# Kernel tuning notes

Measured on AMD Instinct MI355X. Metric: run time of the kernel, lower is better.

Reference implementation:

```python
import jax, jax.numpy as jnp
import numpy as np

C = 256
E = C // 2  # embed_dim = in_channels / 2


def setup_inputs() -> dict:
    key = jax.random.key(0)
    ks = jax.random.split(key, 9)
    B, H, W = 8, 64, 64
    x = jax.random.normal(ks[0], (B, C, H, W), dtype=jnp.float32)
    s_in = 1.0 / np.sqrt(C)
    s_e = 1.0 / np.sqrt(E)
    wq = jax.random.uniform(ks[1], (E, C), jnp.float32, -s_in, s_in)
    bq = jax.random.uniform(ks[2], (E,), jnp.float32, -s_in, s_in)
    wk = jax.random.uniform(ks[3], (E, C), jnp.float32, -s_in, s_in)
    bk = jax.random.uniform(ks[4], (E,), jnp.float32, -s_in, s_in)
    wv = jax.random.uniform(ks[5], (E, C), jnp.float32, -s_in, s_in)
    bv = jax.random.uniform(ks[6], (E,), jnp.float32, -s_in, s_in)
    wo = jax.random.uniform(ks[7], (C, E), jnp.float32, -s_e, s_e)
    bo = jax.random.uniform(ks[8], (C,), jnp.float32, -s_e, s_e)
    return {"x": x, "wq": wq, "bq": bq, "wk": wk, "bk": bk,
            "wv": wv, "bv": bv, "wo": wo, "bo": bo}


def reference(x, wq, bq, wk, bk, wv, bv, wo, bo):
    B, Cc, H, W = x.shape
    N = H * W
    # flatten spatial: [B, N, C]; 1x1 conv == per-pixel linear over channels
    xf = x.reshape(B, Cc, N).transpose(0, 2, 1)
    q = jnp.einsum('bnc,ec->bne', xf, wq) + bq   # [B, N, E]
    k = jnp.einsum('bnc,ec->bne', xf, wk) + bk   # [B, N, E]
    v = jnp.einsum('bnc,ec->bne', xf, wv) + bv   # [B, N, E]
    attn_score = jnp.einsum('bne,bme->bnm', q, k)  # [B, N, N]
    attn_prob = jax.nn.softmax(attn_score, axis=-1)
    feat = jnp.einsum('bnm,bme->bne', attn_prob, v)  # [B, N, E]
    out = jnp.einsum('bne,ce->bnc', feat, wo) + bo   # expansion 1x1 conv
    out = out.transpose(0, 2, 1).reshape(B, Cc, H, W)
    return out + x
```

## Files before the change

kernel.cpp:

```cpp
#include <hip/hip_runtime.h>
#include <hip/hip_bf16.h>


typedef __attribute__((ext_vector_type(8))) short s16x8;
typedef __attribute__((ext_vector_type(4))) short s16x4;
typedef __attribute__((ext_vector_type(4))) float f32x4;

#define B_ 8
#define C_ 256
#define E_ 128
#define N_ 4096
#define SLICES 4
#define SLICE_KV (N_ / SLICES)
#define NTILES (SLICE_KV / 64)
#define PST 76
#define LOG2E 1.44269504f
#define SHIFT2 21.6404256f

#define GLDS16(g, l) __builtin_amdgcn_global_load_lds( \
    (const __attribute__((address_space(1))) void*)(g), \
    (__attribute__((address_space(3))) void*)(l), 16, 0, 0)

static __device__ __forceinline__ unsigned short f2bf(float f) {
    union { float f; unsigned int u; } v; v.f = f;
    return (unsigned short)((v.u + 0x7FFFu + ((v.u >> 16) & 1u)) >> 16);
}
static __device__ __forceinline__ float bf2f(unsigned short h) {
    union { unsigned int u; float f; } v; v.u = ((unsigned int)h) << 16;
    return v.f;
}

__global__ __launch_bounds__(256) void convert_w(
    const float* __restrict__ wq, const float* __restrict__ wk,
    const float* __restrict__ wv, const float* __restrict__ wo,
    unsigned short* __restrict__ wqb, unsigned short* __restrict__ wkb,
    unsigned short* __restrict__ wvb, unsigned short* __restrict__ wob)
{
    const int i = blockIdx.x * 256 + threadIdx.x;
    wqb[i] = f2bf(wq[i]);
    wkb[i] = f2bf(wk[i]);
    wvb[i] = f2bf(wv[i]);
    wob[i] = f2bf(wo[i]);
}

__global__ __launch_bounds__(256, 2) void qkv_kernel(
    const float* __restrict__ x,
    const unsigned short* __restrict__ wqb, const float* __restrict__ bq,
    const unsigned short* __restrict__ wkb, const float* __restrict__ bk,
    const unsigned short* __restrict__ wvb, const float* __restrict__ bv,
    unsigned short* __restrict__ Q, unsigned short* __restrict__ K,
    unsigned short* __restrict__ Vt)
{
    __shared__ unsigned short xs[64 * 264];

    const int tid = threadIdx.x;
    const int b  = blockIdx.x >> 6;
    const int n0 = (blockIdx.x & 63) << 6;

    {
        const int n  = tid & 63;
        const int c0 = tid >> 6;
        const float* xp = x + ((size_t)(b * C_) << 12) + n0 + n;
        for (int it = 0; it < 64; ++it) {
            const int c = it * 4 + c0;
            xs[n * 264 + c] = f2bf(xp[(size_t)c << 12]);
        }
    }
    __syncthreads();

    const int w = tid >> 6, l = tid & 63, hi = l >> 4, lx = l & 15;

    for (int idx = w; idx < 24; idx += 4) {
        const int out = idx >> 3;
        const int et  = idx & 7;
        const int e0  = et << 4;
        const unsigned short* W = (out == 0) ? wqb : (out == 1) ? wkb : wvb;
        const float* bias = (out == 0) ? bq : (out == 1) ? bk : bv;
        const float scale = (out == 0) ? LOG2E : 1.0f;

        s16x8 af[8];
        const unsigned short* wp = W + (e0 + lx) * C_ + hi * 8;
#pragma unroll
        for (int ks = 0; ks < 8; ++ks) af[ks] = *(const s16x8*)(wp + ks * 32);

        float bi[4];
#pragma unroll
        for (int r = 0; r < 4; ++r) bi[r] = bias[e0 + hi * 4 + r];

#pragma unroll
        for (int nt = 0; nt < 4; ++nt) {
            f32x4 acc = {0.f, 0.f, 0.f, 0.f};
#pragma unroll
            for (int ks = 0; ks < 8; ++ks) {
                s16x8 xb = *(const s16x8*)&xs[(nt * 16 + lx) * 264 + ks * 32 + hi * 8];
                acc = __builtin_amdgcn_mfma_f32_16x16x32_bf16(af[ks], xb, acc, 0, 0, 0);
            }
            const int n = n0 + nt * 16 + lx;
            if (out < 2) {
                unsigned short* dst =
                    ((out == 0) ? Q : K) + ((size_t)(b * N_ + n) << 7) + e0 + hi * 4;
                s16x4 pk;
#pragma unroll
                for (int r = 0; r < 4; ++r) pk[r] = (short)f2bf((acc[r] + bi[r]) * scale);
                *(s16x4*)dst = pk;
            } else {
#pragma unroll
                for (int r = 0; r < 4; ++r)
                    Vt[((size_t)(b * E_ + e0 + hi * 4 + r) << 12) + n] =
                        f2bf(acc[r] + bi[r]);
            }
        }
    }
}

__global__ __launch_bounds__(256, 2) void attn_partial(
    const unsigned short* __restrict__ Q, const unsigned short* __restrict__ K,
    const unsigned short* __restrict__ Vt,
    unsigned short* __restrict__ featP, float* __restrict__ denomP)
{
    __shared__ unsigned short Kx[64 * 128];
    __shared__ unsigned short Vs[128 * 64];
    __shared__ unsigned short Ps[4][32 * PST];

    const int tid = threadIdx.x;
    const int b   = blockIdx.x & 7;
    const int idx = blockIdx.x >> 3;
    const int sl  = idx >> 5;
    const int qt  = idx & 31;
    const int w = tid >> 6, l = tid & 63, hi = l >> 4, lx = l & 15;
    const int q0 = qt * 128 + w * 32;

    s16x8 qA[2][4];
#pragma unroll
    for (int qf = 0; qf < 2; ++qf) {
        const unsigned short* qp =
            Q + ((size_t)(b * N_ + q0 + qf * 16 + lx) << 7) + hi * 8;
#pragma unroll
        for (int ks = 0; ks < 4; ++ks) qA[qf][ks] = *(const s16x8*)(qp + ks * 32);
    }

    f32x4 feat[2][8];
#pragma unroll
    for (int qf = 0; qf < 2; ++qf)
#pragma unroll
        for (int ef = 0; ef < 8; ++ef) feat[qf][ef] = (f32x4){0.f, 0.f, 0.f, 0.f};
    float dAcc[8];
#pragma unroll
    for (int i = 0; i < 8; ++i) dAcc[i] = 0.f;

    const unsigned short* Kg = K + ((size_t)(b * N_) << 7);
    const unsigned short* Vg = Vt + ((size_t)(b * E_) << 12);
    unsigned short* pw = &Ps[w][0];


    for (int it = 0; it < NTILES; ++it) {
        const int kv0 = sl * SLICE_KV + it * 64;
        __syncthreads();
#pragma unroll
        for (int i = 0; i < 4; ++i) {
            const int flat = tid + i * 256;
            const int row = flat >> 4, c16 = flat & 15;
            GLDS16(Kg + (size_t)(kv0 + row) * 128 + ((c16 ^ (row & 7)) << 3),
                   &Kx[(i * 256 + w * 64) << 3]);
        }
#pragma unroll
        for (int i = 0; i < 4; ++i) {
            const int flat = tid + i * 256;
            const int e = flat >> 3, c8 = flat & 7;
            GLDS16(Vg + (((size_t)e << 12) + kv0) + ((c8 ^ (e & 7)) << 3),
                   &Vs[(i * 256 + w * 64) << 3]);
        }
        __syncthreads();

#pragma unroll
        for (int kvf = 0; kvf < 4; ++kvf) {
            f32x4 s0 = {0.f, 0.f, 0.f, 0.f}, s1 = {0.f, 0.f, 0.f, 0.f};
#pragma unroll
            for (int ks = 0; ks < 4; ++ks) {
                s16x8 kb = *(const s16x8*)&Kx[((kvf * 16 + lx) << 7) +
                                              (((ks * 4 + hi) ^ (lx & 7)) << 3)];
                s0 = __builtin_amdgcn_mfma_f32_16x16x32_bf16(qA[0][ks], kb, s0, 0, 0, 0);
                s1 = __builtin_amdgcn_mfma_f32_16x16x32_bf16(qA[1][ks], kb, s1, 0, 0, 0);
            }
#pragma unroll
            for (int r = 0; r < 4; ++r) {
                float p0 = __builtin_exp2f(s0[r] - SHIFT2);
                float p1 = __builtin_exp2f(s1[r] - SHIFT2);
                dAcc[r]     += p0;
                dAcc[4 + r] += p1;
                pw[(hi * 4 + r) * PST      + kvf * 16 + lx] = f2bf(p0);
                pw[(16 + hi * 4 + r) * PST + kvf * 16 + lx] = f2bf(p1);
            }
        }
#pragma unroll
        for (int ks = 0; ks < 2; ++ks) {
            s16x8 pa0 = *(const s16x8*)&pw[(lx)      * PST + ks * 32 + hi * 8];
            s16x8 pa1 = *(const s16x8*)&pw[(16 + lx) * PST + ks * 32 + hi * 8];
#pragma unroll
            for (int ef = 0; ef < 8; ++ef) {
                s16x8 vb = *(const s16x8*)&Vs[((ef * 16 + lx) << 6) +
                                              (((ks * 4 + hi) ^ (lx & 7)) << 3)];
                feat[0][ef] = __builtin_amdgcn_mfma_f32_16x16x32_bf16(pa0, vb, feat[0][ef], 0, 0, 0);
                feat[1][ef] = __builtin_amdgcn_mfma_f32_16x16x32_bf16(pa1, vb, feat[1][ef], 0, 0, 0);
            }
        }
    }

#pragma unroll
    for (int i = 0; i < 8; ++i) {
        float v = dAcc[i];
        v += __shfl_xor(v, 1); v += __shfl_xor(v, 2);
        v += __shfl_xor(v, 4); v += __shfl_xor(v, 8);
        dAcc[i] = v;
    }
    const size_t qg = (size_t)((sl * 8 + b) * N_ + q0);
    if (lx == 0) {
        float* dP = denomP + qg;
#pragma unroll
        for (int qf = 0; qf < 2; ++qf)
#pragma unroll
            for (int r = 0; r < 4; ++r)
                dP[qf * 16 + hi * 4 + r] = dAcc[qf * 4 + r];
    }
    unsigned short* fP = featP + (qg << 7);
#pragma unroll
    for (int qf = 0; qf < 2; ++qf)
#pragma unroll
        for (int ef = 0; ef < 8; ++ef)
#pragma unroll
            for (int r = 0; r < 4; ++r)
                fP[(qf * 16 + hi * 4 + r) * 128 + ef * 16 + lx] =
                    f2bf(feat[qf][ef][r]);
}

__global__ __launch_bounds__(256, 2) void combine_kernel(
    const unsigned short* __restrict__ featP, const float* __restrict__ denomP,
    const unsigned short* __restrict__ wob, const float* __restrict__ bo,
    const float* __restrict__ x, float* __restrict__ out)
{
    __shared__ unsigned short fs[64 * 136];

    const int tid = threadIdx.x;
    const int b  = blockIdx.x & 7;
    const int nt = blockIdx.x >> 3;

    {
        const int q = tid >> 2, eb = (tid & 3) * 32;
        const int n = nt * 64 + q;
        float den = 0.f;
#pragma unroll
        for (int s = 0; s < SLICES; ++s)
            den += denomP[(size_t)((s * 8 + b) * N_) + n];
        const float inv = 1.f / den;
#pragma unroll
        for (int e8 = 0; e8 < 4; ++e8) {
            float acc[8];
#pragma unroll
            for (int j = 0; j < 8; ++j) acc[j] = 0.f;
#pragma unroll
            for (int s = 0; s < SLICES; ++s) {
                s16x8 v = *(const s16x8*)(featP +
                    (((size_t)((s * 8 + b) * N_) + n) << 7) + eb + e8 * 8);
#pragma unroll
                for (int j = 0; j < 8; ++j) acc[j] += bf2f((unsigned short)v[j]);
            }
            s16x8 o;
#pragma unroll
            for (int j = 0; j < 8; ++j) o[j] = (short)f2bf(acc[j] * inv);
            *(s16x8*)&fs[q * 136 + eb + e8 * 8] = o;
        }
    }
    __syncthreads();

    const int w = tid >> 6, l = tid & 63, hi = l >> 4, lx = l & 15;

    s16x8 fa[4];
#pragma unroll
    for (int ks = 0; ks < 4; ++ks)
        fa[ks] = *(const s16x8*)&fs[(w * 16 + lx) * 136 + ks * 32 + hi * 8];

    const int n = nt * 64 + w * 16 + lx;
    const float* xb = x + ((size_t)(b * C_) << 12);
    float* ob = out + ((size_t)(b * C_) << 12);
#pragma unroll 1
    for (int ct = 0; ct < 16; ++ct) {
        const unsigned short* wp = wob + (ct * 16 + lx) * 128 + hi * 8;
        f32x4 acc = {0.f, 0.f, 0.f, 0.f};
#pragma unroll
        for (int ks = 0; ks < 4; ++ks) {
            s16x8 wb = *(const s16x8*)(wp + ks * 32);
            acc = __builtin_amdgcn_mfma_f32_16x16x32_bf16(wb, fa[ks], acc, 0, 0, 0);
        }
#pragma unroll
        for (int r = 0; r < 4; ++r) {
            const int c = ct * 16 + hi * 4 + r;
            const size_t off = ((size_t)c << 12) + n;
            ob[off] = acc[r] + bo[c] + xb[off];
        }
    }
}

extern "C" void kernel_launch(void* const* d_in, const int* in_sizes, int n_in,
                              void* d_out, int out_size, void* d_ws, size_t ws_size,
                              hipStream_t stream) {
    (void)in_sizes; (void)n_in; (void)out_size; (void)ws_size;
    const float* x  = (const float*)d_in[0];
    const float* wq = (const float*)d_in[1];
    const float* bq = (const float*)d_in[2];
    const float* wk = (const float*)d_in[3];
    const float* bk = (const float*)d_in[4];
    const float* wv = (const float*)d_in[5];
    const float* bv = (const float*)d_in[6];
    const float* wo = (const float*)d_in[7];
    const float* bo = (const float*)d_in[8];

    unsigned short* Q  = (unsigned short*)d_ws;
    unsigned short* K  = Q + (size_t)B_ * N_ * E_;
    unsigned short* Vt = K + (size_t)B_ * N_ * E_;
    unsigned short* featP = Vt + (size_t)B_ * N_ * E_;
    float* denomP = (float*)(featP + (size_t)SLICES * B_ * N_ * E_);
    unsigned short* wqb = (unsigned short*)(denomP + (size_t)SLICES * B_ * N_);
    unsigned short* wkb = wqb + E_ * C_;
    unsigned short* wvb = wkb + E_ * C_;
    unsigned short* wob = wvb + E_ * C_;

    convert_w<<<dim3(128), dim3(256), 0, stream>>>(
        wq, wk, wv, wo, wqb, wkb, wvb, wob);
    qkv_kernel<<<dim3(B_ * (N_ / 64)), dim3(256), 0, stream>>>(
        x, wqb, bq, wkb, bk, wvb, bv, Q, K, Vt);
    attn_partial<<<dim3(B_ * 32 * SLICES), dim3(256), 0, stream>>>(
        Q, K, Vt, featP, denomP);
    combine_kernel<<<dim3(B_ * 64), dim3(256), 0, stream>>>(
        featP, denomP, wob, bo, x, (float*)d_out);
}
```

Baseline: 175.8 us.

## Double-buffer K/V tiles via register prefetch and swizzle P scratch layout

Replaces the direct global-to-LDS loads, which sat behind two barriers per tile, with register prefetch of the next K/V tile into a second LDS buffer. The goal is to overlap global memory latency with the QK and PV MFMA work, leaving one barrier per iteration. The padded P scratch (stride 76) is also replaced by a dense stride-64 layout with an XOR swizzle to avoid bank conflicts. The cost is double the K/V LDS footprint and extra vector registers for the prefetch, which may hurt occupancy at two blocks per CU.

```diff
diff --git a/kernel.cpp b/kernel.cpp
--- a/kernel.cpp
+++ b/kernel.cpp
@@ -13,13 +13,8 @@
 #define SLICES 4
 #define SLICE_KV (N_ / SLICES)
 #define NTILES (SLICE_KV / 64)
-#define PST 76
 #define LOG2E 1.44269504f
 #define SHIFT2 21.6404256f
-
-#define GLDS16(g, l) __builtin_amdgcn_global_load_lds( \
-    (const __attribute__((address_space(1))) void*)(g), \
-    (__attribute__((address_space(3))) void*)(l), 16, 0, 0)
 
 static __device__ __forceinline__ unsigned short f2bf(float f) {
     union { float f; unsigned int u; } v; v.f = f;
@@ -118,9 +113,9 @@
     const unsigned short* __restrict__ Vt,
     unsigned short* __restrict__ featP, float* __restrict__ denomP)
 {
-    __shared__ unsigned short Kx[64 * 128];
-    __shared__ unsigned short Vs[128 * 64];
-    __shared__ unsigned short Ps[4][32 * PST];
+    __shared__ unsigned short Ks[2][64 * 128];
+    __shared__ unsigned short Vs[2][128 * 64];
+    __shared__ unsigned short Ps[4][32 * 64];
 
     const int tid = threadIdx.x;
     const int b   = blockIdx.x & 7;
@@ -152,57 +147,91 @@
     const unsigned short* Vg = Vt + ((size_t)(b * E_) << 12);
     unsigned short* pw = &Ps[w][0];
 
+    const int kRow[4] = { tid >> 4, (tid + 256) >> 4, (tid + 512) >> 4, (tid + 768) >> 4 };
+    const int kC16 = tid & 15;
+    const int vE[4]  = { tid >> 3, (tid + 256) >> 3, (tid + 512) >> 3, (tid + 768) >> 3 };
+    const int vC8 = tid & 7;
+
+    s16x8 nk[4], nv[4];
+    {
+        const int kv0 = sl * SLICE_KV;
+#pragma unroll
+        for (int i = 0; i < 4; ++i)
+            nk[i] = *(const s16x8*)(Kg + (size_t)(kv0 + kRow[i]) * 128 + kC16 * 8);
+#pragma unroll
+        for (int i = 0; i < 4; ++i)
+            nv[i] = *(const s16x8*)(Vg + ((size_t)vE[i] << 12) + kv0 + vC8 * 8);
+#pragma unroll
+        for (int i = 0; i < 4; ++i)
+            *(s16x8*)&Ks[0][kRow[i] * 128 + ((kC16 ^ (kRow[i] & 7)) << 3)] = nk[i];
+#pragma unroll
+        for (int i = 0; i < 4; ++i)
+            *(s16x8*)&Vs[0][vE[i] * 64 + ((vC8 ^ (vE[i] & 7)) << 3)] = nv[i];
+    }
+    __syncthreads();
 
     for (int it = 0; it < NTILES; ++it) {
-        const int kv0 = sl * SLICE_KV + it * 64;
-        __syncthreads();
-#pragma unroll
-        for (int i = 0; i < 4; ++i) {
-            const int flat = tid + i * 256;
-            const int row = flat >> 4, c16 = flat & 15;
-            GLDS16(Kg + (size_t)(kv0 + row) * 128 + ((c16 ^ (row & 7)) << 3),
-                   &Kx[(i * 256 + w * 64) << 3]);
-        }
-#pragma unroll
-        for (int i = 0; i < 4; ++i) {
-            const int flat = tid + i * 256;
-            const int e = flat >> 3, c8 = flat & 7;
-            GLDS16(Vg + (((size_t)e << 12) + kv0) + ((c8 ^ (e & 7)) << 3),
-                   &Vs[(i * 256 + w * 64) << 3]);
-        }
-        __syncthreads();
-
+        const int cur = it & 1;
+        const bool pf = (it + 1 < NTILES);
+        if (pf) {
+            const int kvn = sl * SLICE_KV + (it + 1) * 64;
+#pragma unroll
+            for (int i = 0; i < 4; ++i)
+                nk[i] = *(const s16x8*)(Kg + (size_t)(kvn + kRow[i]) * 128 + kC16 * 8);
+#pragma unroll
+            for (int i = 0; i < 4; ++i)
+                nv[i] = *(const s16x8*)(Vg + ((size_t)vE[i] << 12) + kvn + vC8 * 8);
+        }
+
+        const unsigned short* kxb = &Ks[cur][0];
 #pragma unroll
         for (int kvf = 0; kvf < 4; ++kvf) {
+            s16x8 kb[4];
+#pragma unroll
+            for (int ks = 0; ks < 4; ++ks)
+                kb[ks] = *(const s16x8*)&kxb[(kvf * 16 + lx) * 128 +
+                                             (((ks * 4 + hi) ^ (lx & 7)) << 3)];
             f32x4 s0 = {0.f, 0.f, 0.f, 0.f}, s1 = {0.f, 0.f, 0.f, 0.f};
 #pragma unroll
             for (int ks = 0; ks < 4; ++ks) {
-                s16x8 kb = *(const s16x8*)&Kx[((kvf * 16 + lx) << 7) +
-                                              (((ks * 4 + hi) ^ (lx & 7)) << 3)];
-                s0 = __builtin_amdgcn_mfma_f32_16x16x32_bf16(qA[0][ks], kb, s0, 0, 0, 0);
-                s1 = __builtin_amdgcn_mfma_f32_16x16x32_bf16(qA[1][ks], kb, s1, 0, 0, 0);
+                s0 = __builtin_amdgcn_mfma_f32_16x16x32_bf16(qA[0][ks], kb[ks], s0, 0, 0, 0);
+                s1 = __builtin_amdgcn_mfma_f32_16x16x32_bf16(qA[1][ks], kb[ks], s1, 0, 0, 0);
             }
 #pragma unroll
             for (int r = 0; r < 4; ++r) {
+                const int key = ((hi * 4 + r) & 7) << 3;
                 float p0 = __builtin_exp2f(s0[r] - SHIFT2);
                 float p1 = __builtin_exp2f(s1[r] - SHIFT2);
                 dAcc[r]     += p0;
                 dAcc[4 + r] += p1;
-                pw[(hi * 4 + r) * PST      + kvf * 16 + lx] = f2bf(p0);
-                pw[(16 + hi * 4 + r) * PST + kvf * 16 + lx] = f2bf(p1);
-            }
-        }
+                pw[(hi * 4 + r) * 64      + ((kvf * 16 + lx) ^ key)] = f2bf(p0);
+                pw[(16 + hi * 4 + r) * 64 + ((kvf * 16 + lx) ^ key)] = f2bf(p1);
+            }
+        }
+        const unsigned short* vxb = &Vs[cur][0];
 #pragma unroll
         for (int ks = 0; ks < 2; ++ks) {
-            s16x8 pa0 = *(const s16x8*)&pw[(lx)      * PST + ks * 32 + hi * 8];
-            s16x8 pa1 = *(const s16x8*)&pw[(16 + lx) * PST + ks * 32 + hi * 8];
+            const int pkey = (lx & 7) << 3;
+            s16x8 pa0 = *(const s16x8*)&pw[(lx)      * 64 + ((ks * 32 + hi * 8) ^ pkey)];
+            s16x8 pa1 = *(const s16x8*)&pw[(16 + lx) * 64 + ((ks * 32 + hi * 8) ^ pkey)];
 #pragma unroll
             for (int ef = 0; ef < 8; ++ef) {
-                s16x8 vb = *(const s16x8*)&Vs[((ef * 16 + lx) << 6) +
-                                              (((ks * 4 + hi) ^ (lx & 7)) << 3)];
+                s16x8 vb = *(const s16x8*)&vxb[(ef * 16 + lx) * 64 +
+                                               (((ks * 4 + hi) ^ (lx & 7)) << 3)];
                 feat[0][ef] = __builtin_amdgcn_mfma_f32_16x16x32_bf16(pa0, vb, feat[0][ef], 0, 0, 0);
                 feat[1][ef] = __builtin_amdgcn_mfma_f32_16x16x32_bf16(pa1, vb, feat[1][ef], 0, 0, 0);
             }
+        }
+
+        if (pf) {
+            const int nxt = cur ^ 1;
+#pragma unroll
+            for (int i = 0; i < 4; ++i)
+                *(s16x8*)&Ks[nxt][kRow[i] * 128 + ((kC16 ^ (kRow[i] & 7)) << 3)] = nk[i];
+#pragma unroll
+            for (int i = 0; i < 4; ++i)
+                *(s16x8*)&Vs[nxt][vE[i] * 64 + ((vC8 ^ (vE[i] & 7)) << 3)] = nv[i];
+            __syncthreads();
         }
     }
 
```

Result: faster. 155.0 us (-11.9%).
